# Kernel tuning notes

Hardware: AMD Instinct MI355X
Metric: run time of the kernel (lower is better)

The kernel has to match this reference:

```python
import jax, jax.numpy as jnp
import numpy as np
import math


def _lsq(x, s, bit, all_positive):
    # LSQ fake-quant: scale -> clamp -> round (STE) -> dequant
    if all_positive:
        qn, qp = 0.0, float(2 ** bit - 1)
    else:
        qn, qp = -float(2 ** (bit - 1)), float(2 ** (bit - 1) - 1)
    g = 1.0 / math.sqrt(x.size * qp)  # grad-scale factor (static)
    sg = s * g
    s_eff = sg + jax.lax.stop_gradient(s - sg)  # fwd = s, grad scaled by g
    xq = jnp.clip(x / s_eff, qn, qp)
    xq = xq + jax.lax.stop_gradient(jnp.round(xq) - xq)  # round with STE
    return xq * s_eff


def _conv(x, w, stride):
    return jax.lax.conv_general_dilated(
        x, w, window_strides=(stride, stride), padding='VALID',
        dimension_numbers=('NCHW', 'OIHW', 'NCHW'))


def setup_inputs() -> dict:
    key = jax.random.key(0)
    ks = jax.random.split(key, 5)
    B = 65536
    x = jax.random.normal(ks[0], (B, 1, 28, 28), dtype=jnp.float32)
    w1 = jax.random.normal(ks[1], (4, 1, 5, 5), dtype=jnp.float32) * 0.2
    w2 = jax.random.normal(ks[2], (8, 4, 3, 3), dtype=jnp.float32) * 0.2
    fc_w = jax.random.normal(ks[3], (10, 200), dtype=jnp.float32) * 0.07
    fc_b = jax.random.normal(ks[4], (10,), dtype=jnp.float32) * 0.01
    one = jnp.ones((1,), dtype=jnp.float32)
    return {"x": x, "w1": w1, "w2": w2, "fc_w": fc_w, "fc_b": fc_b,
            "s_in": one * 0.05, "s_w1": one * 0.02, "s_a1": one * 0.05,
            "s_w2": one * 0.02, "s_a2": one * 0.05, "s_fc": one * 0.02}


def reference(x, w1, w2, fc_w, fc_b, s_in, s_w1, s_a1, s_w2, s_a2, s_fc):
    x = _lsq(x, s_in, 8, False)
    x = _conv(x, _lsq(w1, s_w1, 8, False), 2)          # [B,4,12,12]
    x = jax.nn.relu(_lsq(x, s_a1, 8, True))
    x = _conv(x, _lsq(w2, s_w2, 8, False), 2)          # [B,8,5,5]
    x = jax.nn.relu(_lsq(x, s_a2, 8, True))
    x = x.reshape(x.shape[0], -1)                      # [B,200]
    return x @ _lsq(fc_w, s_fc, 8, False).T + fc_b     # [B,10]
```

## Files before the change

kernel.cpp:

```cpp
#include <hip/hip_runtime.h>
#include <math.h>

#define G  8
#define NG 8

#if __has_builtin(__builtin_amdgcn_sdot4)
__device__ __forceinline__ int dot4(unsigned a, unsigned b, int c) {
    return __builtin_amdgcn_sdot4((int)a, (int)b, c, false);
}
#else
__device__ __forceinline__ int dot4(unsigned a, unsigned b, int c) {
    c += (int)(signed char)(a & 255u)         * (int)(signed char)(b & 255u);
    c += (int)(signed char)((a >> 8) & 255u)  * (int)(signed char)((b >> 8) & 255u);
    c += (int)(signed char)((a >> 16) & 255u) * (int)(signed char)((b >> 16) & 255u);
    c += (int)(signed char)(a >> 24)          * (int)(signed char)(b >> 24);
    return c;
}
#endif

__device__ __forceinline__ void wave_fence() {
    asm volatile("s_waitcnt lgkmcnt(0)" ::: "memory");
}

__device__ __forceinline__ float seff(float s, float gf) {
    float sg = s * gf;
    return sg + (s - sg);
}
__device__ __forceinline__ unsigned q8(float v, float s, float rs) {
    float q0 = v * rs;
    float r  = fmaf(-s, q0, v);
    float y  = fmaf(r, rs, q0);
    y = fminf(fmaxf(y, -128.f), 127.f);
    float t = y + 12582912.0f;
    return __float_as_uint(t);
}
__device__ __forceinline__ unsigned pack4(unsigned a, unsigned b, unsigned c, unsigned d) {
    return (a & 255u) | ((b & 255u) << 8) | ((c & 255u) << 16) | (d << 24);
}
__device__ __forceinline__ int mround(int acc, double r) {
    double t = fma((double)acc, r, 6755399441055744.0);
    return (int)__double_as_longlong(t);
}


extern "C" __global__ __launch_bounds__(256, 4)
void qcnn_fused(const float* __restrict__ x,  const float* __restrict__ w1,
                const float* __restrict__ w2, const float* __restrict__ fcw,
                const float* __restrict__ fcb,
                const float* __restrict__ s_in, const float* __restrict__ s_w1,
                const float* __restrict__ s_a1, const float* __restrict__ s_w2,
                const float* __restrict__ s_a2, const float* __restrict__ s_fc,
                float* __restrict__ out, int B,
                float gx, float gw1, float ga1, float gw2, float ga2, float gfc)
{
    __shared__ __align__(16) unsigned xs[2][G*224];
    __shared__ __align__(16) unsigned a1p[G*144];
    __shared__ __align__(16) unsigned a2p[G*50];
    __shared__ __align__(16) unsigned w1pk[4][5][4];
    __shared__ unsigned w2p[8][9];
    __shared__ unsigned fcp[10][50];
    __shared__ int K2s[8];
    __shared__ int K3s[10];
    __shared__ float fcbs[10];

    const int tid = threadIdx.x;
    const int g   = tid >> 5;
    const int t   = tid & 31;

    const float sx  = seff(s_in[0], gx);
    const float sw1 = seff(s_w1[0], gw1);
    const float sa1 = seff(s_a1[0], ga1);
    const float sw2 = seff(s_w2[0], gw2);
    const float sa2 = seff(s_a2[0], ga2);
    const float sfc = seff(s_fc[0], gfc);
    const float rsx = 1.0f / sx;
    const float rw1 = 1.0f / sw1;
    const float rw2 = 1.0f / sw2;
    const float rfc = 1.0f / sfc;
    const double r1 = (double)sx  * (double)sw1 / (double)sa1;
    const double r2 = (double)sa1 * (double)sw2 / (double)sa2;
    const double r3 = (double)sa2 * (double)sfc;

    const long long gbase = (long long)blockIdx.x * NG;

    const int c8 = t & 7;
    const int eb = (t >> 3) * 7 + c8 - (c8 > 3 ? 1 : 0);

    float4 Rv0, Rv1, Rv2, Rv3, Rv4, Rv5, Rv6;
    auto stage_load = [&](long long grp) {
        const long long img = grp * G + g;
        if (img >= B) return;
        const float4* xp = (const float4*)x + img * 196;
        Rv0 = xp[eb];        Rv1 = xp[eb + 28];  Rv2 = xp[eb + 56];
        Rv3 = xp[eb + 84];   Rv4 = xp[eb + 112]; Rv5 = xp[eb + 140];
        Rv6 = xp[eb + 168];
    };
    auto stage_write = [&](long long grp, int buf) {
        const long long img = grp * G + g;
        if (img >= B) return;
        unsigned* dst = &xs[buf][g*224];
        float4 v;
        v = Rv0; dst[t]       = pack4(q8(v.x,sx,rsx), q8(v.y,sx,rsx), q8(v.z,sx,rsx), q8(v.w,sx,rsx));
        v = Rv1; dst[t + 32]  = pack4(q8(v.x,sx,rsx), q8(v.y,sx,rsx), q8(v.z,sx,rsx), q8(v.w,sx,rsx));
        v = Rv2; dst[t + 64]  = pack4(q8(v.x,sx,rsx), q8(v.y,sx,rsx), q8(v.z,sx,rsx), q8(v.w,sx,rsx));
        v = Rv3; dst[t + 96]  = pack4(q8(v.x,sx,rsx), q8(v.y,sx,rsx), q8(v.z,sx,rsx), q8(v.w,sx,rsx));
        v = Rv4; dst[t + 128] = pack4(q8(v.x,sx,rsx), q8(v.y,sx,rsx), q8(v.z,sx,rsx), q8(v.w,sx,rsx));
        v = Rv5; dst[t + 160] = pack4(q8(v.x,sx,rsx), q8(v.y,sx,rsx), q8(v.z,sx,rsx), q8(v.w,sx,rsx));
        v = Rv6; dst[t + 192] = pack4(q8(v.x,sx,rsx), q8(v.y,sx,rsx), q8(v.z,sx,rsx), q8(v.w,sx,rsx));
    };

    stage_load(gbase);

    if (tid < 80) {
        const int c = tid / 20, rem = tid % 20, ky = rem >> 2, vv = rem & 3;
        const float* wr = w1 + c*25 + ky*5;
        unsigned b[5];
        #pragma unroll
        for (int k = 0; k < 5; ++k) b[k] = q8(wr[k], sw1, rw1) & 255u;
        unsigned pk;
        if      (vv == 0) pk = b[0] | (b[1] << 8) | (b[2] << 16) | (b[3] << 24);
        else if (vv == 1) pk = b[4];
        else if (vv == 2) pk = (b[0] << 16) | (b[1] << 24);
        else              pk = b[2] | (b[3] << 8) | (b[4] << 16);
        w1pk[c][ky][vv] = pk;
    } else if (tid < 152) {
        const int d = tid - 80, oc = d / 9, tap = d % 9;
        unsigned pk = 0;
        #pragma unroll
        for (int ic = 0; ic < 4; ++ic)
            pk |= (q8(w2[oc*36 + ic*9 + tap], sw2, rw2) & 255u) << (8*ic);
        w2p[oc][tap] = pk;
    }
    if (tid < 10) fcbs[tid] = fcb[tid];
    for (int i = tid; i < 500; i += 256) {
        const int o = i / 50, kd = i % 50;
        const float* fr = fcw + o*200 + kd*4;
        fcp[o][kd] = pack4(q8(fr[0],sfc,rfc), q8(fr[1],sfc,rfc),
                           q8(fr[2],sfc,rfc), q8(fr[3],sfc,rfc));
    }
    __syncthreads();
    if (tid < 8) {
        int s = 0;
        #pragma unroll
        for (int d = 0; d < 9; ++d) s = dot4(w2p[tid][d], 0x01010101u, s);
        K2s[tid] = s << 7;
    } else if (tid < 18) {
        const int o = tid - 8;
        int s = 0;
        for (int d = 0; d < 50; ++d) s = dot4(fcp[o][d], 0x01010101u, s);
        K3s[o] = s << 7;
    }
    __syncthreads();
    stage_write(gbase, 0);
    wave_fence();

    int cur = 0;
    for (int it = 0; it < NG; ++it) {
        const long long grp = gbase + it;
        if (grp * G >= B) break;
        const bool act = (grp * G + g) < B;

        if (it + 1 < NG) stage_load(grp + 1);

        if (act) {
            const int c  = t & 3;
            const int h  = (t >> 2) & 1;
            const int y0 = t >> 3;
            uint4 W[5];
            #pragma unroll
            for (int ky = 0; ky < 5; ++ky)
                W[ky] = *(const uint4*)&w1pk[c][ky][0];
            const unsigned* xb = &xs[cur][g*224];
            #pragma unroll
            for (int k = 0; k < 3; ++k) {
                const int y = y0 + 4*k;
                int acc[6] = {0,0,0,0,0,0};
                #pragma unroll
                for (int ky = 0; ky < 5; ++ky) {
                    const uint4 R = *(const uint4*)&xb[(2*y + ky)*8 + 4*h];
                    acc[0] = dot4(R.y, W[ky].y, dot4(R.x, W[ky].x, acc[0]));
                    acc[1] = dot4(R.y, W[ky].w, dot4(R.x, W[ky].z, acc[1]));
                    acc[2] = dot4(R.z, W[ky].y, dot4(R.y, W[ky].x, acc[2]));
                    acc[3] = dot4(R.z, W[ky].w, dot4(R.y, W[ky].z, acc[3]));
                    acc[4] = dot4(R.w, W[ky].y, dot4(R.z, W[ky].x, acc[4]));
                    acc[5] = dot4(R.w, W[ky].w, dot4(R.z, W[ky].z, acc[5]));
                }
                unsigned char* dst = (unsigned char*)a1p + (g*144 + y*12 + 6*h)*4 + c;
                #pragma unroll
                for (int m = 0; m < 6; ++m) {
                    int q = mround(acc[m], r1);
                    q = min(max(q, 0), 255);
                    dst[4*m] = (unsigned char)(q - 128);
                }
            }
        }
        wave_fence();

        if (act) {
            const int oc = t >> 2;
            unsigned wv[9];
            #pragma unroll
            for (int d = 0; d < 9; ++d) wv[d] = w2p[oc][d];
            const int k2 = K2s[oc];
            const unsigned* base = &a1p[g*144];
            unsigned char* dstb = (unsigned char*)a2p + g*200 + oc*25;
            #pragma unroll
            for (int pass = 0; pass < 2; ++pass) {
                const int y = pass ? 4 : (t & 3);
                if (pass && (t & 3) != 0) break;
                unsigned rw[3][12];
                #pragma unroll
                for (int ky = 0; ky < 3; ++ky) {
                    const uint4* rp = (const uint4*)&base[(2*y + ky)*12];
                    uint4 A = rp[0], Bv = rp[1], Cv = rp[2];
                    rw[ky][0]=A.x;  rw[ky][1]=A.y;  rw[ky][2]=A.z;  rw[ky][3]=A.w;
                    rw[ky][4]=Bv.x; rw[ky][5]=Bv.y; rw[ky][6]=Bv.z; rw[ky][7]=Bv.w;
                    rw[ky][8]=Cv.x; rw[ky][9]=Cv.y; rw[ky][10]=Cv.z; rw[ky][11]=Cv.w;
                }
                #pragma unroll
                for (int jx = 0; jx < 5; ++jx) {
                    int acc = k2;
                    #pragma unroll
                    for (int ky = 0; ky < 3; ++ky)
                        #pragma unroll
                        for (int kx = 0; kx < 3; ++kx)
                            acc = dot4(rw[ky][2*jx + kx], wv[ky*3 + kx], acc);
                    int q = mround(acc, r2);
                    q = min(max(q, 0), 255);
                    dstb[y*5 + jx] = (unsigned char)(q - 128);
                }
            }
        }
        wave_fence();

        if (act && t < 30) {
            const int part = t / 10;
            const int o    = t - part*10;
            const int k0   = part * 17;
            const int nk   = (part == 2) ? 16 : 17;
            int acc = 0;
            for (int ki = 0; ki < nk; ++ki) {
                const int k = k0 + ki;
                acc = dot4(a2p[g*50 + k], fcp[o][k], acc);
            }
            const int self0 = (g & 1) * 32 + o;
            const int s1 = __shfl(acc, self0 + 10);
            const int s2 = __shfl(acc, self0 + 20);
            if (part == 0) {
                const int total = acc + s1 + s2 + K3s[o];
                const double oo = (double)total * r3 + (double)fcbs[o];
                out[(grp*G + g)*10 + o] = (float)oo;
            }
        }

        if (it + 1 < NG) {
            stage_write(grp + 1, cur ^ 1);
            wave_fence();
        }
        cur ^= 1;
    }
}

extern "C" void kernel_launch(void* const* d_in, const int* in_sizes, int n_in,
                              void* d_out, int out_size, void* d_ws, size_t ws_size,
                              hipStream_t stream) {
    const float* x    = (const float*)d_in[0];
    const float* w1   = (const float*)d_in[1];
    const float* w2   = (const float*)d_in[2];
    const float* fcw  = (const float*)d_in[3];
    const float* fcb  = (const float*)d_in[4];
    const float* s_in = (const float*)d_in[5];
    const float* s_w1 = (const float*)d_in[6];
    const float* s_a1 = (const float*)d_in[7];
    const float* s_w2 = (const float*)d_in[8];
    const float* s_a2 = (const float*)d_in[9];
    const float* s_fc = (const float*)d_in[10];

    const int B = in_sizes[0] / 784;
    const float gx  = (float)(1.0 / sqrt((double)B * 784.0 * 127.0));
    const float gw1 = (float)(1.0 / sqrt(100.0 * 127.0));
    const float ga1 = (float)(1.0 / sqrt((double)B * 576.0 * 255.0));
    const float gw2 = (float)(1.0 / sqrt(288.0 * 127.0));
    const float ga2 = (float)(1.0 / sqrt((double)B * 200.0 * 255.0));
    const float gfc = (float)(1.0 / sqrt(2000.0 * 127.0));

    const int imgs_per_block = G * NG;
    const int grid = (B + imgs_per_block - 1) / imgs_per_block;
    qcnn_fused<<<grid, 256, 0, stream>>>(x, w1, w2, fcw, fcb,
                                         s_in, s_w1, s_a1, s_w2, s_a2, s_fc,
                                         (float*)d_out, B,
                                         gx, gw1, ga1, gw2, ga2, gfc);
}
```

Measured before the change: 55.27 us.

## Software-pipeline conv1, conv2 and FC stages across groups with double-buffered LDS

Each wave now works on three batch groups at once: conv1 runs on group it, conv2 on group it-1 and the FC layer on group it-2. The a1p and a2p LDS buffers are double-buffered to make this safe, and the loop runs two extra iterations to drain the pipeline. Two of the three per-iteration LDS wait fences are removed, so the stages can overlap and hide latency. The cost is more LDS per block and two drain iterations. The FC stage reads a2p[it&1] where conv2 wrote it at (it-1)&1, which is the same parity and so appears consistent.

```diff
diff --git a/kernel.cpp b/kernel.cpp
--- a/kernel.cpp
+++ b/kernel.cpp
@@ -54,8 +54,8 @@
                 float gx, float gw1, float ga1, float gw2, float ga2, float gfc)
 {
     __shared__ __align__(16) unsigned xs[2][G*224];
-    __shared__ __align__(16) unsigned a1p[G*144];
-    __shared__ __align__(16) unsigned a2p[G*50];
+    __shared__ __align__(16) unsigned a1p[2][G*144];
+    __shared__ __align__(16) unsigned a2p[2][G*50];
     __shared__ __align__(16) unsigned w1pk[4][5][4];
     __shared__ unsigned w2p[8][9];
     __shared__ unsigned fcp[10][50];
@@ -154,15 +154,12 @@
     stage_write(gbase, 0);
     wave_fence();
 
-    int cur = 0;
-    for (int it = 0; it < NG; ++it) {
+    for (int it = 0; it < NG + 2; ++it) {
         const long long grp = gbase + it;
-        if (grp * G >= B) break;
-        const bool act = (grp * G + g) < B;
 
         if (it + 1 < NG) stage_load(grp + 1);
 
-        if (act) {
+        if (it < NG && (grp * G + g) < B) {
             const int c  = t & 3;
             const int h  = (t >> 2) & 1;
             const int y0 = t >> 3;
@@ -170,7 +167,8 @@
             #pragma unroll
             for (int ky = 0; ky < 5; ++ky)
                 W[ky] = *(const uint4*)&w1pk[c][ky][0];
-            const unsigned* xb = &xs[cur][g*224];
+            const unsigned* xb = &xs[it & 1][g*224];
+            unsigned char* a1b = (unsigned char*)&a1p[it & 1][0];
             #pragma unroll
             for (int k = 0; k < 3; ++k) {
                 const int y = y0 + 4*k;
@@ -185,7 +183,7 @@
                     acc[4] = dot4(R.w, W[ky].y, dot4(R.z, W[ky].x, acc[4]));
                     acc[5] = dot4(R.w, W[ky].w, dot4(R.z, W[ky].z, acc[5]));
                 }
-                unsigned char* dst = (unsigned char*)a1p + (g*144 + y*12 + 6*h)*4 + c;
+                unsigned char* dst = a1b + (g*144 + y*12 + 6*h)*4 + c;
                 #pragma unroll
                 for (int m = 0; m < 6; ++m) {
                     int q = mround(acc[m], r1);
@@ -194,16 +192,15 @@
                 }
             }
         }
-        wave_fence();
-
-        if (act) {
+
+        if (it >= 1 && it <= NG && ((grp - 1) * G + g) < B) {
             const int oc = t >> 2;
             unsigned wv[9];
             #pragma unroll
             for (int d = 0; d < 9; ++d) wv[d] = w2p[oc][d];
             const int k2 = K2s[oc];
-            const unsigned* base = &a1p[g*144];
-            unsigned char* dstb = (unsigned char*)a2p + g*200 + oc*25;
+            const unsigned* base = &a1p[(it - 1) & 1][g*144];
+            unsigned char* dstb = (unsigned char*)&a2p[(it - 1) & 1][0] + g*200 + oc*25;
             #pragma unroll
             for (int pass = 0; pass < 2; ++pass) {
                 const int y = pass ? 4 : (t & 3);
@@ -231,17 +228,17 @@
                 }
             }
         }
-        wave_fence();
-
-        if (act && t < 30) {
+
+        if (it >= 2 && ((grp - 2) * G + g) < B && t < 30) {
             const int part = t / 10;
             const int o    = t - part*10;
             const int k0   = part * 17;
             const int nk   = (part == 2) ? 16 : 17;
+            const unsigned* a2b = &a2p[it & 1][g*50];
             int acc = 0;
             for (int ki = 0; ki < nk; ++ki) {
                 const int k = k0 + ki;
-                acc = dot4(a2p[g*50 + k], fcp[o][k], acc);
+                acc = dot4(a2b[k], fcp[o][k], acc);
             }
             const int self0 = (g & 1) * 32 + o;
             const int s1 = __shfl(acc, self0 + 10);
@@ -249,15 +246,13 @@
             if (part == 0) {
                 const int total = acc + s1 + s2 + K3s[o];
                 const double oo = (double)total * r3 + (double)fcbs[o];
-                out[(grp*G + g)*10 + o] = (float)oo;
+                out[((grp - 2)*G + g)*10 + o] = (float)oo;
             }
         }
 
-        if (it + 1 < NG) {
-            stage_write(grp + 1, cur ^ 1);
-            wave_fence();
-        }
-        cur ^= 1;
+        if (it + 1 < NG) stage_write(grp + 1, (it + 1) & 1);
+
+        wave_fence();
     }
 }
 
```

Result: no change. 55.53 us (+0.5%).

## Drop register prefetch pipeline, raise occupancy, pad LDS rows, vectorize FC dot

Applied to the files above, without the earlier changes.

Removes the register double-buffered input prefetch and the second LDS input buffer. Each wave now loads and quantizes its image at the start of every iteration. Launch bounds rise to 8 blocks per CU and each block handles 4 groups instead of 8, so occupancy rather than software pipelining hides global latency. The input rows are padded to 12 words, conv2 accumulates row by row without staging a 3x12 register array, and the FC layer uses padded, aligned uint4 LDS loads. The cost is lost explicit load/compute overlap inside a wave, plus a larger grid and more per-block setup.

```diff
diff --git a/kernel.cpp b/kernel.cpp
--- a/kernel.cpp
+++ b/kernel.cpp
@@ -2,7 +2,7 @@
 #include <math.h>
 
 #define G  8
-#define NG 8
+#define NG 4
 
 #if __has_builtin(__builtin_amdgcn_sdot4)
 __device__ __forceinline__ int dot4(unsigned a, unsigned b, int c) {
@@ -43,7 +43,7 @@
 }
 
 
-extern "C" __global__ __launch_bounds__(256, 4)
+extern "C" __global__ __launch_bounds__(256, 8)
 void qcnn_fused(const float* __restrict__ x,  const float* __restrict__ w1,
                 const float* __restrict__ w2, const float* __restrict__ fcw,
                 const float* __restrict__ fcb,
@@ -53,12 +53,12 @@
                 float* __restrict__ out, int B,
                 float gx, float gw1, float ga1, float gw2, float ga2, float gfc)
 {
-    __shared__ __align__(16) unsigned xs[2][G*224];
+    __shared__ __align__(16) unsigned xs[G*336];
     __shared__ __align__(16) unsigned a1p[G*144];
-    __shared__ __align__(16) unsigned a2p[G*50];
+    __shared__ __align__(16) unsigned a2p[G*52];
     __shared__ __align__(16) unsigned w1pk[4][5][4];
     __shared__ unsigned w2p[8][9];
-    __shared__ unsigned fcp[10][50];
+    __shared__ __align__(16) unsigned fcp[10][52];
     __shared__ int K2s[8];
     __shared__ int K3s[10];
     __shared__ float fcbs[10];
@@ -85,31 +85,7 @@
 
     const int c8 = t & 7;
     const int eb = (t >> 3) * 7 + c8 - (c8 > 3 ? 1 : 0);
-
-    float4 Rv0, Rv1, Rv2, Rv3, Rv4, Rv5, Rv6;
-    auto stage_load = [&](long long grp) {
-        const long long img = grp * G + g;
-        if (img >= B) return;
-        const float4* xp = (const float4*)x + img * 196;
-        Rv0 = xp[eb];        Rv1 = xp[eb + 28];  Rv2 = xp[eb + 56];
-        Rv3 = xp[eb + 84];   Rv4 = xp[eb + 112]; Rv5 = xp[eb + 140];
-        Rv6 = xp[eb + 168];
-    };
-    auto stage_write = [&](long long grp, int buf) {
-        const long long img = grp * G + g;
-        if (img >= B) return;
-        unsigned* dst = &xs[buf][g*224];
-        float4 v;
-        v = Rv0; dst[t]       = pack4(q8(v.x,sx,rsx), q8(v.y,sx,rsx), q8(v.z,sx,rsx), q8(v.w,sx,rsx));
-        v = Rv1; dst[t + 32]  = pack4(q8(v.x,sx,rsx), q8(v.y,sx,rsx), q8(v.z,sx,rsx), q8(v.w,sx,rsx));
-        v = Rv2; dst[t + 64]  = pack4(q8(v.x,sx,rsx), q8(v.y,sx,rsx), q8(v.z,sx,rsx), q8(v.w,sx,rsx));
-        v = Rv3; dst[t + 96]  = pack4(q8(v.x,sx,rsx), q8(v.y,sx,rsx), q8(v.z,sx,rsx), q8(v.w,sx,rsx));
-        v = Rv4; dst[t + 128] = pack4(q8(v.x,sx,rsx), q8(v.y,sx,rsx), q8(v.z,sx,rsx), q8(v.w,sx,rsx));
-        v = Rv5; dst[t + 160] = pack4(q8(v.x,sx,rsx), q8(v.y,sx,rsx), q8(v.z,sx,rsx), q8(v.w,sx,rsx));
-        v = Rv6; dst[t + 192] = pack4(q8(v.x,sx,rsx), q8(v.y,sx,rsx), q8(v.z,sx,rsx), q8(v.w,sx,rsx));
-    };
-
-    stage_load(gbase);
+    const int db = (t >> 3) * 12 + c8;
 
     if (tid < 80) {
         const int c = tid / 20, rem = tid % 20, ky = rem >> 2, vv = rem & 3;
@@ -151,16 +127,23 @@
         K3s[o] = s << 7;
     }
     __syncthreads();
-    stage_write(gbase, 0);
-    wave_fence();
-
-    int cur = 0;
+
     for (int it = 0; it < NG; ++it) {
         const long long grp = gbase + it;
         if (grp * G >= B) break;
         const bool act = (grp * G + g) < B;
 
-        if (it + 1 < NG) stage_load(grp + 1);
+        if (act) {
+            const float4* xp = (const float4*)x + (grp * G + g) * 196;
+            unsigned* dst = &xs[g*336];
+            #pragma unroll 2
+            for (int k = 0; k < 7; ++k) {
+                float4 v = xp[eb + 28*k];
+                dst[db + 48*k] = pack4(q8(v.x,sx,rsx), q8(v.y,sx,rsx),
+                                       q8(v.z,sx,rsx), q8(v.w,sx,rsx));
+            }
+        }
+        wave_fence();
 
         if (act) {
             const int c  = t & 3;
@@ -170,14 +153,14 @@
             #pragma unroll
             for (int ky = 0; ky < 5; ++ky)
                 W[ky] = *(const uint4*)&w1pk[c][ky][0];
-            const unsigned* xb = &xs[cur][g*224];
+            const unsigned* xb = &xs[g*336];
             #pragma unroll
             for (int k = 0; k < 3; ++k) {
                 const int y = y0 + 4*k;
                 int acc[6] = {0,0,0,0,0,0};
                 #pragma unroll
                 for (int ky = 0; ky < 5; ++ky) {
-                    const uint4 R = *(const uint4*)&xb[(2*y + ky)*8 + 4*h];
+                    const uint4 R = *(const uint4*)&xb[(2*y + ky)*12 + 4*h];
                     acc[0] = dot4(R.y, W[ky].y, dot4(R.x, W[ky].x, acc[0]));
                     acc[1] = dot4(R.y, W[ky].w, dot4(R.x, W[ky].z, acc[1]));
                     acc[2] = dot4(R.z, W[ky].y, dot4(R.y, W[ky].x, acc[2]));
@@ -203,29 +186,29 @@
             for (int d = 0; d < 9; ++d) wv[d] = w2p[oc][d];
             const int k2 = K2s[oc];
             const unsigned* base = &a1p[g*144];
-            unsigned char* dstb = (unsigned char*)a2p + g*200 + oc*25;
+            unsigned char* dstb = (unsigned char*)a2p + g*208 + oc*25;
             #pragma unroll
             for (int pass = 0; pass < 2; ++pass) {
                 const int y = pass ? 4 : (t & 3);
                 if (pass && (t & 3) != 0) break;
-                unsigned rw[3][12];
+                int acc[5] = {k2, k2, k2, k2, k2};
                 #pragma unroll
                 for (int ky = 0; ky < 3; ++ky) {
                     const uint4* rp = (const uint4*)&base[(2*y + ky)*12];
                     uint4 A = rp[0], Bv = rp[1], Cv = rp[2];
-                    rw[ky][0]=A.x;  rw[ky][1]=A.y;  rw[ky][2]=A.z;  rw[ky][3]=A.w;
-                    rw[ky][4]=Bv.x; rw[ky][5]=Bv.y; rw[ky][6]=Bv.z; rw[ky][7]=Bv.w;
-                    rw[ky][8]=Cv.x; rw[ky][9]=Cv.y; rw[ky][10]=Cv.z; rw[ky][11]=Cv.w;
+                    const unsigned rw[12] = {A.x,A.y,A.z,A.w,
+                                             Bv.x,Bv.y,Bv.z,Bv.w,
+                                             Cv.x,Cv.y,Cv.z,Cv.w};
+                    #pragma unroll
+                    for (int jx = 0; jx < 5; ++jx) {
+                        acc[jx] = dot4(rw[2*jx],     wv[ky*3],     acc[jx]);
+                        acc[jx] = dot4(rw[2*jx + 1], wv[ky*3 + 1], acc[jx]);
+                        acc[jx] = dot4(rw[2*jx + 2], wv[ky*3 + 2], acc[jx]);
+                    }
                 }
                 #pragma unroll
                 for (int jx = 0; jx < 5; ++jx) {
-                    int acc = k2;
-                    #pragma unroll
-                    for (int ky = 0; ky < 3; ++ky)
-                        #pragma unroll
-                        for (int kx = 0; kx < 3; ++kx)
-                            acc = dot4(rw[ky][2*jx + kx], wv[ky*3 + kx], acc);
-                    int q = mround(acc, r2);
+                    int q = mround(acc[jx], r2);
                     q = min(max(q, 0), 255);
                     dstb[y*5 + jx] = (unsigned char)(q - 128);
                 }
@@ -236,12 +219,20 @@
         if (act && t < 30) {
             const int part = t / 10;
             const int o    = t - part*10;
-            const int k0   = part * 17;
-            const int nk   = (part == 2) ? 16 : 17;
+            const int k0   = part << 4;
+            const unsigned* a2b = &a2p[g*52];
+            const uint4* ap = (const uint4*)(a2b + k0);
+            const uint4* wp = (const uint4*)(&fcp[o][0] + k0);
             int acc = 0;
-            for (int ki = 0; ki < nk; ++ki) {
-                const int k = k0 + ki;
-                acc = dot4(a2p[g*50 + k], fcp[o][k], acc);
+            #pragma unroll
+            for (int q4 = 0; q4 < 4; ++q4) {
+                uint4 a = ap[q4], w = wp[q4];
+                acc = dot4(a.x, w.x, acc); acc = dot4(a.y, w.y, acc);
+                acc = dot4(a.z, w.z, acc); acc = dot4(a.w, w.w, acc);
+            }
+            if (part == 2) {
+                acc = dot4(a2b[48], fcp[o][48], acc);
+                acc = dot4(a2b[49], fcp[o][49], acc);
             }
             const int self0 = (g & 1) * 32 + o;
             const int s1 = __shfl(acc, self0 + 10);
@@ -252,12 +243,7 @@
                 out[(grp*G + g)*10 + o] = (float)oo;
             }
         }
-
-        if (it + 1 < NG) {
-            stage_write(grp + 1, cur ^ 1);
-            wave_fence();
-        }
-        cur ^= 1;
+        wave_fence();
     }
 }
 
```

Result: slower. 62.81 us (+13.6%).
